# Optimization experiments

Hardware: AMD Instinct MI355X
Metric: run time of the kernel (lower is better)

The kernel has to match this reference:

```python
import jax, jax.numpy as jnp
import numpy as np

IMG = 448; P = 16; C = 3; D = 512; DC = 8; DS = 4
NH = IMG // P            # 28 patches per side
NPATCH = NH * NH         # 784
PDIM = C * P * P         # 768
BATCH = 32
EPS = 1e-5


def setup_inputs() -> dict:
    key = jax.random.key(0)
    ks = jax.random.split(key, 10)
    def lin(k, fan_in, shape):
        bound = 1.0 / np.sqrt(fan_in)
        return jax.random.uniform(k, shape, jnp.float32, -bound, bound)
    return {
        "images": jax.random.normal(ks[0], (BATCH, C, IMG, IMG), jnp.float32),
        "W_patch": lin(ks[1], PDIM, (PDIM, D)),
        "b_patch": jnp.zeros((D,), jnp.float32),
        "pos_embed": jax.random.normal(ks[2], (1, NPATCH, D), jnp.float32) * 0.02,
        "W_coord": lin(ks[3], D, (D, DC)),
        "b_coord": jnp.zeros((DC,), jnp.float32),
        "W_spinor": lin(ks[4], D, (D, DS)),
        "b_spinor": jnp.zeros((DS,), jnp.float32),
        "W_embed": lin(ks[5], DC, (DC, D)),
        "b_embed": jnp.zeros((D,), jnp.float32),
        "ln_gamma": jnp.ones((D,), jnp.float32),
        "ln_beta": jnp.zeros((D,), jnp.float32),
        "W_out": lin(ks[6], D, (D, D)),
        "b_out": jnp.zeros((D,), jnp.float32),
    }


def reference(images, W_patch, b_patch, pos_embed, W_coord, b_coord,
              W_spinor, b_spinor, W_embed, b_embed,
              ln_gamma, ln_beta, W_out, b_out):
    B = images.shape[0]
    # patchify == F.unfold(kernel=stride=P).transpose(1,2):
    # patches[b, bh*NH+bw, c*P*P + i*P + j] = images[b, c, bh*P+i, bw*P+j]
    patches = images.reshape(B, C, NH, P, NH, P)
    patches = patches.transpose(0, 2, 4, 1, 3, 5).reshape(B, NPATCH, PDIM)
    # patch embed + positional embedding  -> (B, NPATCH, D)
    x = patches @ W_patch + b_patch + pos_embed
    # manifold projection: coords (B,N,DC), spinor (B,N,DS)
    coords = x @ W_coord + b_coord
    spinor = x @ W_spinor + b_spinor
    # K0 scalar bilinear: psi^T psi -> (B, N)
    K0 = jnp.sum(spinor * spinor, axis=-1)
    # embed back from manifold coords -> (B, N, D)
    x_manifold = coords @ W_embed + b_embed
    # K0-modulated remix + residual
    x_enh = x_manifold * K0[..., None] + x
    # output projection: LayerNorm -> Linear
    mu = jnp.mean(x_enh, axis=-1, keepdims=True)
    var = jnp.mean(jnp.square(x_enh - mu), axis=-1, keepdims=True)
    x_norm = (x_enh - mu) * jax.lax.rsqrt(var + EPS) * ln_gamma + ln_beta
    return x_norm @ W_out + b_out
```

## Files before the change

kernel.cpp:

```cpp
#include <hip/hip_runtime.h>
#include <hip/hip_bf16.h>
#include <stdint.h>


typedef __bf16 bf16_t;
typedef bf16_t bf16x8 __attribute__((ext_vector_type(8)));
typedef bf16_t bf16x4 __attribute__((ext_vector_type(4)));
typedef float  f32x4  __attribute__((ext_vector_type(4)));

#define IMG     448
#define PSZ     16
#define NHP     28
#define NPATCH  784
#define PDIM    768
#define DMODEL  512
#define MROWS   25088

__device__ __forceinline__ void gload16(void* lds, const void* g) {
  __builtin_amdgcn_global_load_lds(
      (__attribute__((address_space(1))) void*)(uintptr_t)g,
      (__attribute__((address_space(3))) void*)lds,
      16, 0, 0);
}

__global__ __launch_bounds__(256) void transpose_to_bf16(
    const float* __restrict__ src, bf16_t* __restrict__ dst, int K, int N)
{
  __shared__ float t[64][65];
  const int tx = threadIdx.x;
  const int ty = threadIdx.y;
  const int bx = blockIdx.x * 64;
  const int by = blockIdx.y * 64;
  #pragma unroll
  for (int r = ty; r < 64; r += 4)
    t[r][tx] = src[(size_t)(by + r) * N + (bx + tx)];
  __syncthreads();
  #pragma unroll
  for (int r = ty; r < 64; r += 4)
    dst[(size_t)(bx + r) * K + (by + tx)] = (bf16_t)t[tx][r];
}

__global__ __launch_bounds__(256) void manifold_prep(
    const float* __restrict__ Wc, const float* __restrict__ Ws,
    bf16_t* __restrict__ Wcsg)
{
  const int idx = blockIdx.x * 256 + threadIdx.x;
  if (idx < 8192) {
    const int r = idx >> 9, n = idx & 511;
    float v = 0.f;
    if (r < 8)       v = Wc[n * 8 + r];
    else if (r < 12) v = Ws[n * 4 + (r - 8)];
    Wcsg[idx] = (bf16_t)v;
  }
}

__global__ __launch_bounds__(256) void patchify_bf16(
    const float* __restrict__ images, bf16_t* __restrict__ Apat)
{
  __shared__ bf16_t t[16][456];
  const int tid = threadIdx.x;
  const int bid = blockIdx.x;
  const int b = bid / 84, rem = bid % 84;
  const int c = rem / 28, ph = rem % 28;
  const float* src = images + ((size_t)(b * 3 + c) * IMG + ph * PSZ) * IMG;

  #pragma unroll
  for (int idx = tid; idx < 16 * 112; idx += 256) {
    const int i = idx / 112, x4 = idx % 112;
    const float4 v = *(const float4*)(src + (size_t)i * IMG + x4 * 4);
    bf16x4 w;
    w[0] = (bf16_t)v.x; w[1] = (bf16_t)v.y; w[2] = (bf16_t)v.z; w[3] = (bf16_t)v.w;
    *(bf16x4*)&t[i][x4 * 4] = w;
  }
  __syncthreads();

  const size_t mbase = (size_t)b * NPATCH + (size_t)ph * NHP;
  #pragma unroll
  for (int idx = tid; idx < 28 * 64; idx += 256) {
    const int pw = idx >> 6, e = idx & 63;
    const int i = e >> 2, j4 = e & 3;
    const bf16x4 w = *(const bf16x4*)&t[i][pw * 16 + j4 * 4];
    *(bf16x4*)&Apat[(mbase + pw) * PDIM + c * 256 + i * 16 + j4 * 4] = w;
  }
}

template<int KDIM, int EPI>
__global__ __launch_bounds__(256) void gemm_bf16(
    const bf16_t* __restrict__ A, const bf16_t* __restrict__ BT,
    const float* __restrict__ bias, const float* __restrict__ pos,
    void* __restrict__ outp)
{
  __shared__ bf16_t As[64 * 64];
  __shared__ bf16_t Bs[64 * 64];
  constexpr int NT = KDIM / 64;

  const int tid  = threadIdx.x;
  const int orig = blockIdx.x;
  const int wg   = (orig & 7) * 392 + (orig >> 3);
  const int n0   = (wg & 7) * 64;
  const int m0   = (wg >> 3) * 64;

  const int wave = tid >> 6, lane = tid & 63;

  const int ra = lane >> 3;
  const int ca = (lane & 7) ^ ra;
  const bf16_t* ag = A  + (size_t)(m0 + wave * 8 + ra) * KDIM + ca * 8;
  const bf16_t* bg = BT + (size_t)(n0 + wave * 8 + ra) * KDIM + ca * 8;
  bf16_t* al0 = As + (wave * 8) * 64;
  bf16_t* al1 = As + (wave * 8 + 32) * 64;
  bf16_t* bl0 = Bs + (wave * 8) * 64;
  bf16_t* bl1 = Bs + (wave * 8 + 32) * 64;

  const int wm = (wave >> 1) * 32;
  const int wn = (wave & 1) * 32;
  const int lr = lane & 15;
  const int lt = lane >> 4;

  f32x4 acc[2][2] = {};

  for (int t = 0; t < NT; ++t) {
    const int k0 = t * 64;
    __syncthreads();
    gload16(al0, ag + k0);
    gload16(al1, ag + 32 * KDIM + k0);
    gload16(bl0, bg + k0);
    gload16(bl1, bg + 32 * KDIM + k0);
    __syncthreads();

    #pragma unroll
    for (int ks = 0; ks < 2; ++ks) {
      const int c = ks * 4 + lt;
      bf16x8 af[2], bfr[2];
      #pragma unroll
      for (int i = 0; i < 2; ++i) {
        const int row = wm + i * 16 + lr;
        af[i] = *(const bf16x8*)&As[row * 64 + ((c ^ (row & 7)) * 8)];
      }
      #pragma unroll
      for (int j = 0; j < 2; ++j) {
        const int row = wn + j * 16 + lr;
        bfr[j] = *(const bf16x8*)&Bs[row * 64 + ((c ^ (row & 7)) * 8)];
      }
      #pragma unroll
      for (int i = 0; i < 2; ++i)
        #pragma unroll
        for (int j = 0; j < 2; ++j)
          acc[i][j] = __builtin_amdgcn_mfma_f32_16x16x32_bf16(af[i], bfr[j], acc[i][j], 0, 0, 0);
    }
  }

  const int q4 = lt << 2;
  const int colb = n0 + wn;
  #pragma unroll
  for (int i = 0; i < 2; ++i) {
    #pragma unroll
    for (int r = 0; r < 4; ++r) {
      const int mm = m0 + wm + i * 16 + q4 + r;
      if (EPI == 0) {
        const int pp = mm % NPATCH;
        const float* pe = pos + (size_t)pp * DMODEL;
        bf16_t* orow = (bf16_t*)outp + (size_t)mm * DMODEL;
        #pragma unroll
        for (int j = 0; j < 2; ++j) {
          const int nn = colb + j * 16 + lr;
          orow[nn] = (bf16_t)(acc[i][j][r] + bias[nn] + pe[nn]);
        }
      } else {
        float* orow = (float*)outp + (size_t)mm * DMODEL;
        #pragma unroll
        for (int j = 0; j < 2; ++j) {
          const int nn = colb + j * 16 + lr;
          orow[nn] = acc[i][j][r] + bias[nn];
        }
      }
    }
  }
}

__global__ __launch_bounds__(64) void manifold_v5(
    bf16_t* __restrict__ x, const bf16_t* __restrict__ Wcsg,
    const float* __restrict__ b_coord, const float* __restrict__ b_spinor,
    const float* __restrict__ We, const float* __restrict__ be,
    const float* __restrict__ gamma, const float* __restrict__ beta)
{
  __shared__ float cbuf[16][12];

  const int lane = threadIdx.x;
  const int lr   = lane & 15;
  const int lk   = (lane >> 4) << 3;
  const int q4   = (lane >> 4) << 2;
  const int m0w  = blockIdx.x * 16;

  float bbv[4];
  #pragma unroll
  for (int r = 0; r < 4; ++r) {
    if (q4 == 0)      bbv[r] = b_coord[r];
    else if (q4 == 4) bbv[r] = b_coord[4 + r];
    else if (q4 == 8) bbv[r] = b_spinor[r];
    else              bbv[r] = 0.f;
  }

  const bf16_t* xrow = x + (size_t)(m0w + lr) * DMODEL + lk;
  const bf16_t* wrow = Wcsg + lr * DMODEL + lk;
  f32x4 acc1 = {0.f, 0.f, 0.f, 0.f};
  #pragma unroll
  for (int ks = 0; ks < 16; ++ks) {
    const bf16x8 bf = *(const bf16x8*)(xrow + ks * 32);
    const bf16x8 wf = *(const bf16x8*)(wrow + ks * 32);
    acc1 = __builtin_amdgcn_mfma_f32_16x16x32_bf16(wf, bf, acc1, 0, 0, 0);
  }
  float sv[4];
  #pragma unroll
  for (int r = 0; r < 4; ++r) sv[r] = acc1[r] + bbv[r];

  if (q4 == 8) {
    cbuf[lr][8] = sv[0] * sv[0] + sv[1] * sv[1] + sv[2] * sv[2] + sv[3] * sv[3];
  } else if (q4 == 0 || q4 == 4) {
    f32x4 st = {sv[0], sv[1], sv[2], sv[3]};
    *(f32x4*)&cbuf[lr][q4] = st;
  }
  __syncthreads();

  const int n0 = lane * 8;
  f32x4 wlo[8], whi[8];
  #pragma unroll
  for (int dc = 0; dc < 8; ++dc) {
    wlo[dc] = *(const f32x4*)&We[dc * DMODEL + n0];
    whi[dc] = *(const f32x4*)&We[dc * DMODEL + n0 + 4];
  }
  const f32x4 beL = *(const f32x4*)&be[n0];
  const f32x4 beH = *(const f32x4*)&be[n0 + 4];
  const f32x4 gL  = *(const f32x4*)&gamma[n0];
  const f32x4 gH  = *(const f32x4*)&gamma[n0 + 4];
  const f32x4 btL = *(const f32x4*)&beta[n0];
  const f32x4 btH = *(const f32x4*)&beta[n0 + 4];

  #pragma unroll 2
  for (int rr = 0; rr < 16; ++rr) {
    const size_t row = (size_t)m0w + rr;
    const bf16x8 xv = *(const bf16x8*)(x + row * DMODEL + n0);
    const f32x4 c0 = *(const f32x4*)&cbuf[rr][0];
    const f32x4 c1 = *(const f32x4*)&cbuf[rr][4];
    const float k0 = cbuf[rr][8];

    float v[8];
    float s1 = 0.f, s2 = 0.f;
    #pragma unroll
    for (int e = 0; e < 4; ++e) {
      float xm = beL[e];
      #pragma unroll
      for (int dc = 0; dc < 4; ++dc) xm += c0[dc] * wlo[dc][e];
      #pragma unroll
      for (int dc = 0; dc < 4; ++dc) xm += c1[dc] * wlo[4 + dc][e];
      const float vv = xm * k0 + (float)xv[e];
      v[e] = vv; s1 += vv; s2 += vv * vv;
    }
    #pragma unroll
    for (int e = 0; e < 4; ++e) {
      float xm = beH[e];
      #pragma unroll
      for (int dc = 0; dc < 4; ++dc) xm += c0[dc] * whi[dc][e];
      #pragma unroll
      for (int dc = 0; dc < 4; ++dc) xm += c1[dc] * whi[4 + dc][e];
      const float vv = xm * k0 + (float)xv[4 + e];
      v[4 + e] = vv; s1 += vv; s2 += vv * vv;
    }

    #pragma unroll
    for (int off = 1; off <= 32; off <<= 1) {
      s1 += __shfl_xor(s1, off, 64);
      s2 += __shfl_xor(s2, off, 64);
    }
    const float mu  = s1 * (1.f / 512.f);
    const float var = s2 * (1.f / 512.f) - mu * mu;
    const float rs  = rsqrtf(var + 1e-5f);

    bf16x8 o;
    #pragma unroll
    for (int e = 0; e < 4; ++e) {
      o[e]     = (bf16_t)((v[e]     - mu) * rs * gL[e] + btL[e]);
      o[4 + e] = (bf16_t)((v[4 + e] - mu) * rs * gH[e] + btH[e]);
    }
    *(bf16x8*)(x + row * DMODEL + n0) = o;
  }
}

extern "C" void kernel_launch(void* const* d_in, const int* in_sizes, int n_in,
                              void* d_out, int out_size, void* d_ws, size_t ws_size,
                              hipStream_t stream)
{
  const float* images    = (const float*)d_in[0];
  const float* W_patch   = (const float*)d_in[1];
  const float* b_patch   = (const float*)d_in[2];
  const float* pos_embed = (const float*)d_in[3];
  const float* W_coord   = (const float*)d_in[4];
  const float* b_coord   = (const float*)d_in[5];
  const float* W_spinor  = (const float*)d_in[6];
  const float* b_spinor  = (const float*)d_in[7];
  const float* W_embed   = (const float*)d_in[8];
  const float* b_embed   = (const float*)d_in[9];
  const float* ln_gamma  = (const float*)d_in[10];
  const float* ln_beta   = (const float*)d_in[11];
  const float* W_out     = (const float*)d_in[12];
  const float* b_out     = (const float*)d_in[13];
  float* out = (float*)d_out;

  const size_t SZ_APAT = (size_t)MROWS * PDIM * 2;
  const size_t SZ_X    = (size_t)MROWS * DMODEL * 2;
  const size_t SZ_WPT  = (size_t)DMODEL * PDIM * 2;
  const size_t SZ_WOT  = (size_t)DMODEL * DMODEL * 2;

  char* ws = (char*)d_ws;
  char* p  = ws;
  bf16_t* Apat = (bf16_t*)p;   p += SZ_APAT;
  bf16_t* x    = (bf16_t*)p;   p += SZ_X;
  bf16_t* WpT  = (bf16_t*)p;   p += SZ_WPT;
  bf16_t* WoT  = (bf16_t*)p;   p += SZ_WOT;
  bf16_t* Wcsg = (bf16_t*)p;

  hipLaunchKernelGGL(transpose_to_bf16, dim3(8, 12), dim3(64, 4), 0, stream,
                     W_patch, WpT, PDIM, DMODEL);
  hipLaunchKernelGGL(transpose_to_bf16, dim3(8, 8), dim3(64, 4), 0, stream,
                     W_out, WoT, DMODEL, DMODEL);
  hipLaunchKernelGGL(manifold_prep, dim3(32), dim3(256), 0, stream,
                     W_coord, W_spinor, Wcsg);

  hipLaunchKernelGGL(patchify_bf16, dim3(32 * 3 * 28), dim3(256), 0, stream,
                     images, Apat);
  hipLaunchKernelGGL((gemm_bf16<PDIM, 0>), dim3(3136), dim3(256), 0, stream,
                     Apat, WpT, b_patch, pos_embed, (void*)x);

  hipLaunchKernelGGL(manifold_v5, dim3(MROWS / 16), dim3(64), 0, stream,
                     x, Wcsg, b_coord, b_spinor, W_embed, b_embed, ln_gamma, ln_beta);

  hipLaunchKernelGGL((gemm_bf16<DMODEL, 1>), dim3(3136), dim3(256), 0, stream,
                     x, WoT, b_out, (const float*)nullptr, (void*)out);
}
```

Measured before the change: 114.2 us.

## Widen GEMM tiles to 64x128, split manifold K-reduction across waves, merge prep kernels

The GEMM block tile grows from 64x64 to 64x128, so each wave computes 32x64 outputs with 8 MFMA accumulators and A tiles get more reuse, at the cost of half the blocks and more registers. The manifold kernel moves to 256-thread blocks handling 32 rows. The K=512 reduction is split across two wave halves with partial sums combined in LDS, and each wave then normalizes 8 rows. The three weight-prep kernels are merged into one launch to cut launch overhead.

```diff
diff --git a/kernel.cpp b/kernel.cpp
--- a/kernel.cpp
+++ b/kernel.cpp
@@ -23,14 +23,34 @@
       16, 0, 0);
 }
 
-__global__ __launch_bounds__(256) void transpose_to_bf16(
-    const float* __restrict__ src, bf16_t* __restrict__ dst, int K, int N)
+__global__ __launch_bounds__(256) void prep_all(
+    const float* __restrict__ Wp, const float* __restrict__ Wo,
+    const float* __restrict__ Wc, const float* __restrict__ Ws,
+    bf16_t* __restrict__ WpT, bf16_t* __restrict__ WoT,
+    bf16_t* __restrict__ Wcsg)
 {
   __shared__ float t[64][65];
-  const int tx = threadIdx.x;
-  const int ty = threadIdx.y;
-  const int bx = blockIdx.x * 64;
-  const int by = blockIdx.y * 64;
+  const int tid = threadIdx.x;
+  const int blk = blockIdx.x;
+
+  if (blk >= 160) {
+    for (int idx = tid; idx < 8192; idx += 256) {
+      const int r = idx >> 9, n = idx & 511;
+      float v = 0.f;
+      if (r < 8)       v = Wc[n * 8 + r];
+      else if (r < 12) v = Ws[n * 4 + (r - 8)];
+      Wcsg[idx] = (bf16_t)v;
+    }
+    return;
+  }
+
+  const float* src;  bf16_t* dst;  int K, N, bx, by;
+  if (blk < 96) { src = Wp; dst = WpT; K = PDIM;   N = DMODEL;
+                  bx = (blk & 7) * 64;        by = (blk >> 3) * 64; }
+  else          { src = Wo; dst = WoT; K = DMODEL; N = DMODEL;
+                  bx = ((blk - 96) & 7) * 64; by = ((blk - 96) >> 3) * 64; }
+
+  const int tx = tid & 63, ty = tid >> 6;
   #pragma unroll
   for (int r = ty; r < 64; r += 4)
     t[r][tx] = src[(size_t)(by + r) * N + (bx + tx)];
@@ -38,20 +58,6 @@
   #pragma unroll
   for (int r = ty; r < 64; r += 4)
     dst[(size_t)(bx + r) * K + (by + tx)] = (bf16_t)t[tx][r];
-}
-
-__global__ __launch_bounds__(256) void manifold_prep(
-    const float* __restrict__ Wc, const float* __restrict__ Ws,
-    bf16_t* __restrict__ Wcsg)
-{
-  const int idx = blockIdx.x * 256 + threadIdx.x;
-  if (idx < 8192) {
-    const int r = idx >> 9, n = idx & 511;
-    float v = 0.f;
-    if (r < 8)       v = Wc[n * 8 + r];
-    else if (r < 12) v = Ws[n * 4 + (r - 8)];
-    Wcsg[idx] = (bf16_t)v;
-  }
 }
 
 __global__ __launch_bounds__(256) void patchify_bf16(
@@ -91,14 +97,14 @@
     void* __restrict__ outp)
 {
   __shared__ bf16_t As[64 * 64];
-  __shared__ bf16_t Bs[64 * 64];
+  __shared__ bf16_t Bs[128 * 64];
   constexpr int NT = KDIM / 64;
 
   const int tid  = threadIdx.x;
   const int orig = blockIdx.x;
-  const int wg   = (orig & 7) * 392 + (orig >> 3);
-  const int n0   = (wg & 7) * 64;
-  const int m0   = (wg >> 3) * 64;
+  const int wg   = (orig & 7) * 196 + (orig >> 3);
+  const int n0   = (wg & 3) * 128;
+  const int m0   = (wg >> 2) * 64;
 
   const int wave = tid >> 6, lane = tid & 63;
 
@@ -110,13 +116,15 @@
   bf16_t* al1 = As + (wave * 8 + 32) * 64;
   bf16_t* bl0 = Bs + (wave * 8) * 64;
   bf16_t* bl1 = Bs + (wave * 8 + 32) * 64;
+  bf16_t* bl2 = Bs + (wave * 8 + 64) * 64;
+  bf16_t* bl3 = Bs + (wave * 8 + 96) * 64;
 
   const int wm = (wave >> 1) * 32;
-  const int wn = (wave & 1) * 32;
+  const int wn = (wave & 1) * 64;
   const int lr = lane & 15;
   const int lt = lane >> 4;
 
-  f32x4 acc[2][2] = {};
+  f32x4 acc[2][4] = {};
 
   for (int t = 0; t < NT; ++t) {
     const int k0 = t * 64;
@@ -125,26 +133,28 @@
     gload16(al1, ag + 32 * KDIM + k0);
     gload16(bl0, bg + k0);
     gload16(bl1, bg + 32 * KDIM + k0);
+    gload16(bl2, bg + 64 * KDIM + k0);
+    gload16(bl3, bg + 96 * KDIM + k0);
     __syncthreads();
 
     #pragma unroll
     for (int ks = 0; ks < 2; ++ks) {
       const int c = ks * 4 + lt;
-      bf16x8 af[2], bfr[2];
+      bf16x8 af[2], bfr[4];
       #pragma unroll
       for (int i = 0; i < 2; ++i) {
         const int row = wm + i * 16 + lr;
         af[i] = *(const bf16x8*)&As[row * 64 + ((c ^ (row & 7)) * 8)];
       }
       #pragma unroll
-      for (int j = 0; j < 2; ++j) {
+      for (int j = 0; j < 4; ++j) {
         const int row = wn + j * 16 + lr;
         bfr[j] = *(const bf16x8*)&Bs[row * 64 + ((c ^ (row & 7)) * 8)];
       }
       #pragma unroll
       for (int i = 0; i < 2; ++i)
         #pragma unroll
-        for (int j = 0; j < 2; ++j)
+        for (int j = 0; j < 4; ++j)
           acc[i][j] = __builtin_amdgcn_mfma_f32_16x16x32_bf16(af[i], bfr[j], acc[i][j], 0, 0, 0);
     }
   }
@@ -161,14 +171,14 @@
         const float* pe = pos + (size_t)pp * DMODEL;
         bf16_t* orow = (bf16_t*)outp + (size_t)mm * DMODEL;
         #pragma unroll
-        for (int j = 0; j < 2; ++j) {
+        for (int j = 0; j < 4; ++j) {
           const int nn = colb + j * 16 + lr;
           orow[nn] = (bf16_t)(acc[i][j][r] + bias[nn] + pe[nn]);
         }
       } else {
         float* orow = (float*)outp + (size_t)mm * DMODEL;
         #pragma unroll
-        for (int j = 0; j < 2; ++j) {
+        for (int j = 0; j < 4; ++j) {
           const int nn = colb + j * 16 + lr;
           orow[nn] = acc[i][j][r] + bias[nn];
         }
@@ -177,47 +187,36 @@
   }
 }
 
-__global__ __launch_bounds__(64) void manifold_v5(
+__global__ __launch_bounds__(256) void manifold_v6(
     bf16_t* __restrict__ x, const bf16_t* __restrict__ Wcsg,
     const float* __restrict__ b_coord, const float* __restrict__ b_spinor,
     const float* __restrict__ We, const float* __restrict__ be,
     const float* __restrict__ gamma, const float* __restrict__ beta)
 {
-  __shared__ float cbuf[16][12];
-
-  const int lane = threadIdx.x;
+  __shared__ float pbuf[2][2][16][12];
+
+  const int tid  = threadIdx.x;
+  const int w    = tid >> 6;
+  const int lane = tid & 63;
+  const int rg   = w & 1;
+  const int kh   = w >> 1;
   const int lr   = lane & 15;
   const int lk   = (lane >> 4) << 3;
   const int q4   = (lane >> 4) << 2;
-  const int m0w  = blockIdx.x * 16;
-
-  float bbv[4];
-  #pragma unroll
-  for (int r = 0; r < 4; ++r) {
-    if (q4 == 0)      bbv[r] = b_coord[r];
-    else if (q4 == 4) bbv[r] = b_coord[4 + r];
-    else if (q4 == 8) bbv[r] = b_spinor[r];
-    else              bbv[r] = 0.f;
-  }
-
-  const bf16_t* xrow = x + (size_t)(m0w + lr) * DMODEL + lk;
-  const bf16_t* wrow = Wcsg + lr * DMODEL + lk;
+  const size_t mbase = (size_t)blockIdx.x * 32;
+
+  const bf16_t* xrow = x + (mbase + rg * 16 + lr) * DMODEL + kh * 256 + lk;
+  const bf16_t* wrow = Wcsg + lr * DMODEL + kh * 256 + lk;
   f32x4 acc1 = {0.f, 0.f, 0.f, 0.f};
   #pragma unroll
-  for (int ks = 0; ks < 16; ++ks) {
+  for (int ks = 0; ks < 8; ++ks) {
     const bf16x8 bf = *(const bf16x8*)(xrow + ks * 32);
     const bf16x8 wf = *(const bf16x8*)(wrow + ks * 32);
     acc1 = __builtin_amdgcn_mfma_f32_16x16x32_bf16(wf, bf, acc1, 0, 0, 0);
   }
-  float sv[4];
-  #pragma unroll
-  for (int r = 0; r < 4; ++r) sv[r] = acc1[r] + bbv[r];
-
-  if (q4 == 8) {
-    cbuf[lr][8] = sv[0] * sv[0] + sv[1] * sv[1] + sv[2] * sv[2] + sv[3] * sv[3];
-  } else if (q4 == 0 || q4 == 4) {
-    f32x4 st = {sv[0], sv[1], sv[2], sv[3]};
-    *(f32x4*)&cbuf[lr][q4] = st;
+  if (q4 < 12) {
+    #pragma unroll
+    for (int r = 0; r < 4; ++r) pbuf[kh][rg][lr][q4 + r] = acc1[r];
   }
   __syncthreads();
 
@@ -234,14 +233,30 @@
   const f32x4 gH  = *(const f32x4*)&gamma[n0 + 4];
   const f32x4 btL = *(const f32x4*)&beta[n0];
   const f32x4 btH = *(const f32x4*)&beta[n0 + 4];
+  float bc[8], bs[4];
+  #pragma unroll
+  for (int dc = 0; dc < 8; ++dc) bc[dc] = b_coord[dc];
+  #pragma unroll
+  for (int ds = 0; ds < 4; ++ds) bs[ds] = b_spinor[ds];
 
   #pragma unroll 2
-  for (int rr = 0; rr < 16; ++rr) {
-    const size_t row = (size_t)m0w + rr;
+  for (int rr = 0; rr < 8; ++rr) {
+    const int rloc = w * 8 + rr;
+    const int rg2  = rloc >> 4, r16 = rloc & 15;
+    const float* p0 = &pbuf[0][rg2][r16][0];
+    const float* p1 = &pbuf[1][rg2][r16][0];
+    float c[8];
+    #pragma unroll
+    for (int dc = 0; dc < 8; ++dc) c[dc] = p0[dc] + p1[dc] + bc[dc];
+    float k0 = 0.f;
+    #pragma unroll
+    for (int ds = 0; ds < 4; ++ds) {
+      const float s = p0[8 + ds] + p1[8 + ds] + bs[ds];
+      k0 += s * s;
+    }
+
+    const size_t row = mbase + rloc;
     const bf16x8 xv = *(const bf16x8*)(x + row * DMODEL + n0);
-    const f32x4 c0 = *(const f32x4*)&cbuf[rr][0];
-    const f32x4 c1 = *(const f32x4*)&cbuf[rr][4];
-    const float k0 = cbuf[rr][8];
 
     float v[8];
     float s1 = 0.f, s2 = 0.f;
@@ -249,9 +264,7 @@
     for (int e = 0; e < 4; ++e) {
       float xm = beL[e];
       #pragma unroll
-      for (int dc = 0; dc < 4; ++dc) xm += c0[dc] * wlo[dc][e];
-      #pragma unroll
-      for (int dc = 0; dc < 4; ++dc) xm += c1[dc] * wlo[4 + dc][e];
+      for (int dc = 0; dc < 8; ++dc) xm += c[dc] * wlo[dc][e];
       const float vv = xm * k0 + (float)xv[e];
       v[e] = vv; s1 += vv; s2 += vv * vv;
     }
@@ -259,9 +272,7 @@
     for (int e = 0; e < 4; ++e) {
       float xm = beH[e];
       #pragma unroll
-      for (int dc = 0; dc < 4; ++dc) xm += c0[dc] * whi[dc][e];
-      #pragma unroll
-      for (int dc = 0; dc < 4; ++dc) xm += c1[dc] * whi[4 + dc][e];
+      for (int dc = 0; dc < 8; ++dc) xm += c[dc] * whi[dc][e];
       const float vv = xm * k0 + (float)xv[4 + e];
       v[4 + e] = vv; s1 += vv; s2 += vv * vv;
     }
@@ -318,21 +329,17 @@
   bf16_t* WoT  = (bf16_t*)p;   p += SZ_WOT;
   bf16_t* Wcsg = (bf16_t*)p;
 
-  hipLaunchKernelGGL(transpose_to_bf16, dim3(8, 12), dim3(64, 4), 0, stream,
-                     W_patch, WpT, PDIM, DMODEL);
-  hipLaunchKernelGGL(transpose_to_bf16, dim3(8, 8), dim3(64, 4), 0, stream,
-                     W_out, WoT, DMODEL, DMODEL);
-  hipLaunchKernelGGL(manifold_prep, dim3(32), dim3(256), 0, stream,
-                     W_coord, W_spinor, Wcsg);
+  hipLaunchKernelGGL(prep_all, dim3(161), dim3(256), 0, stream,
+                     W_patch, W_out, W_coord, W_spinor, WpT, WoT, Wcsg);
 
   hipLaunchKernelGGL(patchify_bf16, dim3(32 * 3 * 28), dim3(256), 0, stream,
                      images, Apat);
-  hipLaunchKernelGGL((gemm_bf16<PDIM, 0>), dim3(3136), dim3(256), 0, stream,
+  hipLaunchKernelGGL((gemm_bf16<PDIM, 0>), dim3(1568), dim3(256), 0, stream,
                      Apat, WpT, b_patch, pos_embed, (void*)x);
 
-  hipLaunchKernelGGL(manifold_v5, dim3(MROWS / 16), dim3(64), 0, stream,
+  hipLaunchKernelGGL(manifold_v6, dim3(MROWS / 32), dim3(256), 0, stream,
                      x, Wcsg, b_coord, b_spinor, W_embed, b_embed, ln_gamma, ln_beta);
 
-  hipLaunchKernelGGL((gemm_bf16<DMODEL, 1>), dim3(3136), dim3(256), 0, stream,
+  hipLaunchKernelGGL((gemm_bf16<DMODEL, 1>), dim3(1568), dim3(256), 0, stream,
                      x, WoT, b_out, (const float*)nullptr, (void*)out);
 }
```

New measurement: 108.2 us. -5.2%, faster.
